# Performance work log

Measured on AMD Instinct MI355X. Metric: run time of the kernel, lower is better.

Reference implementation:

```python
import jax, jax.numpy as jnp
import numpy as np

B, N, E = 4, 4096, 65536
FIN, FOUT = 128, 64
ALPHA = 0.2          # LeakyReLU negative slope
NEG = -9e15          # mask value from original code


def setup_inputs() -> dict:
    key = jax.random.key(0)
    k1, k2, k3, k4 = jax.random.split(key, 4)
    h = jax.random.normal(k1, (B, N, FIN), dtype=jnp.float32)
    edge_index = jax.random.randint(k2, (B, 2, E), 0, N, dtype=jnp.int32)
    # Xavier-uniform-like params
    W = jax.random.uniform(k3, (FIN, FOUT), jnp.float32, -1.0, 1.0) * (1.414 * np.sqrt(6.0 / (FIN + FOUT)))
    a = jax.random.uniform(k4, (2 * FOUT, 1), jnp.float32, -1.0, 1.0) * (1.414 * np.sqrt(6.0 / (2 * FOUT + 1)))
    return {"h": h, "edge_index": edge_index, "W": W, "a": a}


def reference(h, edge_index, W, a):
    # Wh: [B, N, FOUT]
    Wh = jnp.einsum('bnf,fo->bno', h, W)
    Wh_flat = Wh.reshape(-1, FOUT)  # [B*N, FOUT]

    # Faithful to original: raw node ids (< N) index the flattened tensor,
    # i.e. edge features are gathered from batch 0's rows.
    src = edge_index[:, 0].reshape(-1)  # [B*E]
    tgt = edge_index[:, 1].reshape(-1)  # [B*E]
    a_input = jnp.concatenate([Wh_flat[src], Wh_flat[tgt]], axis=1)  # [B*E, 2*FOUT]
    e = (a_input @ a)[:, 0]  # [B*E]

    b_idx = jnp.repeat(jnp.arange(B), E)
    e_dense = jnp.zeros((B, N, N), e.dtype).at[b_idx, src, tgt].set(e)
    e_dense = jax.nn.leaky_relu(e_dense, ALPHA)

    attention = jnp.where(e_dense > 0, e_dense, NEG)
    attention = jax.nn.softmax(attention, axis=1)  # softmax over dim=1 as in original
    # dropout p=0.0 -> no-op

    h_prime = jnp.einsum('bmn,bnf->bmf', attention, Wh)  # [B, N, FOUT]
    return jax.nn.elu(h_prime)  # concat=True path
```

## Files before the change

kernel.cpp:

```cpp
#include <hip/hip_runtime.h>
#include <hip/hip_bf16.h>

#define BB 4
#define NN 4096
#define EE 65536
#define FIN 128
#define FOUT 64
#define CAP 64

__device__ __forceinline__ unsigned enc_f32(float f) {
    unsigned b = __float_as_uint(f);
    return (b & 0x80000000u) ? ~b : (b | 0x80000000u);
}
__device__ __forceinline__ float dec_f32(unsigned e) {
    unsigned b = (e & 0x80000000u) ? (e & 0x7FFFFFFFu) : ~e;
    return __uint_as_float(b);
}

__global__ void init_kernel(const float* __restrict__ W, const float* __restrict__ a,
                            int* __restrict__ deg, unsigned* __restrict__ Menc,
                            float* __restrict__ D, float* __restrict__ base,
                            float* __restrict__ Wa) {
    int tid = threadIdx.x;
    int gid = blockIdx.x * 256 + tid;
    deg[gid] = 0;
    Menc[gid] = 0u;
    D[gid] = 0.f;
    if (gid < BB * FOUT) base[gid] = 0.f;
    if (blockIdx.x == 0) {
        int half = tid >> 7, k = tid & 127;
        const float* wr = W + k * FOUT;
        const float* av = a + half * FOUT;
        float s = 0.f;
#pragma unroll 16
        for (int f = 0; f < FOUT; ++f) s += wr[f] * av[f];
        Wa[half * 128 + k] = s;
    }
}

__global__ void as_at_kernel(const float* __restrict__ h, const float* __restrict__ Wa,
                             float* __restrict__ as_, float* __restrict__ at_) {
    int tid = threadIdx.x;
    int lane = tid & 63;
    int n = blockIdx.x * 4 + (tid >> 6);
    float h0v = h[(long)n * FIN + lane];
    float h1v = h[(long)n * FIN + 64 + lane];
    float ps = h0v * Wa[lane] + h1v * Wa[64 + lane];
    float pt = h0v * Wa[128 + lane] + h1v * Wa[192 + lane];
    for (int off = 32; off; off >>= 1) {
        ps += __shfl_down(ps, off);
        pt += __shfl_down(pt, off);
    }
    if (lane == 0) { as_[n] = ps; at_[n] = pt; }
}

__global__ __launch_bounds__(256) void wh_kernel(const float* __restrict__ h,
                                                 const float* __restrict__ W,
                                                 float* __restrict__ Wh) {
    __shared__ float hs[32][132];
    __shared__ float Ws[128][64];
    int tid = threadIdx.x;
    long row0 = (long)blockIdx.x * 32;
    for (int i = tid; i < 2048; i += 256) {
        float4 v = ((const float4*)W)[i];
        int k = (i * 4) >> 6, c = (i * 4) & 63;
        *(float4*)&Ws[k][c] = v;
    }
    for (int i = tid; i < 1024; i += 256) {
        float4 v = ((const float4*)(h + row0 * FIN))[i];
        int r = (i * 4) >> 7, c = (i * 4) & 127;
        *(float4*)&hs[r][c] = v;
    }
    __syncthreads();
    int tx = tid & 15, ty = tid >> 4;
    int c0 = tx * 4, r0 = ty * 2;
    float acc[2][4] = {};
#pragma unroll
    for (int k = 0; k < 128; k += 4) {
        float4 w0 = *(const float4*)&Ws[k][c0];
        float4 w1 = *(const float4*)&Ws[k + 1][c0];
        float4 w2 = *(const float4*)&Ws[k + 2][c0];
        float4 w3 = *(const float4*)&Ws[k + 3][c0];
#pragma unroll
        for (int r = 0; r < 2; ++r) {
            float4 hv = *(const float4*)&hs[r0 + r][k];
            acc[r][0] += hv.x * w0.x + hv.y * w1.x + hv.z * w2.x + hv.w * w3.x;
            acc[r][1] += hv.x * w0.y + hv.y * w1.y + hv.z * w2.y + hv.w * w3.y;
            acc[r][2] += hv.x * w0.z + hv.y * w1.z + hv.z * w2.z + hv.w * w3.z;
            acc[r][3] += hv.x * w0.w + hv.y * w1.w + hv.z * w2.w + hv.w * w3.w;
        }
    }
#pragma unroll
    for (int r = 0; r < 2; ++r)
        *(float4*)&Wh[(row0 + r0 + r) * FOUT + c0] = *(float4*)&acc[r][0];
}

__global__ void edge_kernel(const int* __restrict__ ei, const float* __restrict__ as_,
                            const float* __restrict__ at_, unsigned* __restrict__ Menc,
                            int* __restrict__ deg, int* __restrict__ csr) {
    int idx = blockIdx.x * 256 + threadIdx.x;
    int b = idx >> 16;
    int j = idx & 65535;
    const int* eb = ei + (long)b * 2 * EE;
    int s = eb[j], t = eb[EE + j];
    float as_s = as_[s];
    float e = as_s + at_[t];
    if (e > 0.f) {
        int row = (b << 12) | s;
        atomicMax(&Menc[(b << 12) | t], enc_f32(as_s));
        int slot = atomicAdd(&deg[row], 1);
        if (slot < CAP) csr[row * CAP + slot] = t;
    }
}

__global__ void dedup_denom_kernel(int* __restrict__ deg, int* __restrict__ csr,
                                   const float* __restrict__ as_,
                                   const unsigned* __restrict__ Menc,
                                   float* __restrict__ D) {
    int tid = threadIdx.x;
    int lane = tid & 63;
    int row = blockIdx.x * 4 + (tid >> 6);
    int b = row >> 12, s = row & 4095;
    int draw = min(deg[row], CAP);
    int t = -1;
    if (lane < draw) t = csr[row * CAP + lane];
    bool dup = false;
    for (int k = 0; k < draw; ++k) {
        int tk = __shfl(t, k);
        if (k < lane && tk == t) dup = true;
    }
    bool keep = (lane < draw) && !dup;
    unsigned long long mask = __ballot(keep);
    int pfx = __popcll(mask & ((1ull << lane) - 1ull));
    if (keep) {
        csr[row * CAP + pfx] = t;
        float M = dec_f32(Menc[(b << 12) | t]);
        atomicAdd(&D[(b << 12) | t], expf(as_[s] - M));
    }
    if (lane == 0) deg[row] = __popcll(mask);
}

__global__ void base_kernel(const unsigned* __restrict__ Menc, const float* __restrict__ Wh,
                            float* __restrict__ base) {
    int bx = blockIdx.x;
    int b = bx >> 5, chunk = bx & 31;
    int f = threadIdx.x & 63, ty = threadIdx.x >> 6;
    float acc = 0.f;
    int t0 = chunk * (NN / 32);
    for (int t = t0 + ty; t < t0 + NN / 32; t += 4)
        if (Menc[(b << 12) | t] == 0u) acc += Wh[(((long)b << 12) | t) * FOUT + f];
    __shared__ float red[4][64];
    red[ty][f] = acc;
    __syncthreads();
    if (ty == 0)
        atomicAdd(&base[(b << 6) | f],
                  (red[0][f] + red[1][f] + red[2][f] + red[3][f]) * (1.0f / NN));
}

__global__ void gather_kernel(const int* __restrict__ deg, const int* __restrict__ csr,
                              const float* __restrict__ as_, const unsigned* __restrict__ Menc,
                              const float* __restrict__ D, const float* __restrict__ Wh,
                              const float* __restrict__ base, float* __restrict__ out) {
    int tid = threadIdx.x;
    int lane = tid & 63;
    int row = blockIdx.x * 4 + (tid >> 6);
    int b = row >> 12, s = row & 4095;
    int d = deg[row];
    float as_s = as_[s];
    float acc = 0.f;
    const int* cr = csr + row * CAP;
    const float* Whb = Wh + (((long)b << 12) * FOUT);
    for (int j = 0; j < d; ++j) {
        int t = cr[j];
        float M = dec_f32(Menc[(b << 12) | t]);
        float w = expf(as_s - M) / D[(b << 12) | t];
        acc += w * Whb[t * FOUT + lane];
    }
    float x = acc + base[(b << 6) | lane];
    out[(long)row * FOUT + lane] = x > 0.f ? x : expm1f(x);
}

extern "C" void kernel_launch(void* const* d_in, const int* in_sizes, int n_in,
                              void* d_out, int out_size, void* d_ws, size_t ws_size,
                              hipStream_t stream) {
    const float* h  = (const float*)d_in[0];
    const int*   ei = (const int*)d_in[1];
    const float* W  = (const float*)d_in[2];
    const float* a  = (const float*)d_in[3];
    float* out = (float*)d_out;

    char* ws = (char*)d_ws;
    float*    Wh   = (float*)(ws);
    int*      csr  = (int*)(ws + 4194304);
    int*      deg  = (int*)(ws + 8388608);
    unsigned* Menc = (unsigned*)(ws + 8454144);
    float*    D    = (float*)(ws + 8519680);
    float*    as_  = (float*)(ws + 8585216);
    float*    at_  = (float*)(ws + 8601600);
    float*    base = (float*)(ws + 8617984);
    float*    Wa   = (float*)(ws + 8619008);

    init_kernel<<<64, 256, 0, stream>>>(W, a, deg, Menc, D, base, Wa);
    wh_kernel<<<BB * NN / 32, 256, 0, stream>>>(h, W, Wh);
    as_at_kernel<<<NN / 4, 256, 0, stream>>>(h, Wa, as_, at_);
    edge_kernel<<<(BB * EE) / 256, 256, 0, stream>>>(ei, as_, at_, Menc, deg, csr);
    dedup_denom_kernel<<<(BB * NN) / 4, 256, 0, stream>>>(deg, csr, as_, Menc, D);
    base_kernel<<<BB * 32, 256, 0, stream>>>(Menc, Wh, base);
    gather_kernel<<<(BB * NN) / 4, 256, 0, stream>>>(deg, csr, as_, Menc, D, Wh, base, out);
}
```

Before: 79.47 us.

## Merge init, Wh and score kernels; fold base reduction into dedup kernel

After: 88.20 us. 1.11x slower.

```diff
diff --git a/kernel.cpp b/kernel.cpp
--- a/kernel.cpp
+++ b/kernel.cpp
@@ -17,82 +17,84 @@
     return __uint_as_float(b);
 }
 
-__global__ void init_kernel(const float* __restrict__ W, const float* __restrict__ a,
-                            int* __restrict__ deg, unsigned* __restrict__ Menc,
-                            float* __restrict__ D, float* __restrict__ base,
-                            float* __restrict__ Wa) {
+__global__ __launch_bounds__(256) void phase0_kernel(
+        const float* __restrict__ h, const float* __restrict__ W, const float* __restrict__ a,
+        float* __restrict__ Wh, int* __restrict__ deg, unsigned* __restrict__ Menc,
+        float* __restrict__ D, float* __restrict__ base,
+        float* __restrict__ as_, float* __restrict__ at_) {
+    __shared__ union {
+        struct { float hs[32][132]; float Ws[64][64]; } wh;
+        float Wa[256];
+    } smem;
     int tid = threadIdx.x;
-    int gid = blockIdx.x * 256 + tid;
-    deg[gid] = 0;
-    Menc[gid] = 0u;
-    D[gid] = 0.f;
-    if (gid < BB * FOUT) base[gid] = 0.f;
-    if (blockIdx.x == 0) {
-        int half = tid >> 7, k = tid & 127;
-        const float* wr = W + k * FOUT;
-        const float* av = a + half * FOUT;
-        float s = 0.f;
-#pragma unroll 16
-        for (int f = 0; f < FOUT; ++f) s += wr[f] * av[f];
-        Wa[half * 128 + k] = s;
-    }
-}
-
-__global__ void as_at_kernel(const float* __restrict__ h, const float* __restrict__ Wa,
-                             float* __restrict__ as_, float* __restrict__ at_) {
-    int tid = threadIdx.x;
-    int lane = tid & 63;
-    int n = blockIdx.x * 4 + (tid >> 6);
-    float h0v = h[(long)n * FIN + lane];
-    float h1v = h[(long)n * FIN + 64 + lane];
-    float ps = h0v * Wa[lane] + h1v * Wa[64 + lane];
-    float pt = h0v * Wa[128 + lane] + h1v * Wa[192 + lane];
-    for (int off = 32; off; off >>= 1) {
-        ps += __shfl_down(ps, off);
-        pt += __shfl_down(pt, off);
-    }
-    if (lane == 0) { as_[n] = ps; at_[n] = pt; }
-}
-
-__global__ __launch_bounds__(256) void wh_kernel(const float* __restrict__ h,
-                                                 const float* __restrict__ W,
-                                                 float* __restrict__ Wh) {
-    __shared__ float hs[32][132];
-    __shared__ float Ws[128][64];
-    int tid = threadIdx.x;
-    long row0 = (long)blockIdx.x * 32;
-    for (int i = tid; i < 2048; i += 256) {
-        float4 v = ((const float4*)W)[i];
-        int k = (i * 4) >> 6, c = (i * 4) & 63;
-        *(float4*)&Ws[k][c] = v;
-    }
-    for (int i = tid; i < 1024; i += 256) {
-        float4 v = ((const float4*)(h + row0 * FIN))[i];
-        int r = (i * 4) >> 7, c = (i * 4) & 127;
-        *(float4*)&hs[r][c] = v;
-    }
-    __syncthreads();
-    int tx = tid & 15, ty = tid >> 4;
-    int c0 = tx * 4, r0 = ty * 2;
-    float acc[2][4] = {};
-#pragma unroll
-    for (int k = 0; k < 128; k += 4) {
-        float4 w0 = *(const float4*)&Ws[k][c0];
-        float4 w1 = *(const float4*)&Ws[k + 1][c0];
-        float4 w2 = *(const float4*)&Ws[k + 2][c0];
-        float4 w3 = *(const float4*)&Ws[k + 3][c0];
+    int bid = blockIdx.x;
+    if (bid < 512) {
+        long row0 = (long)bid * 32;
+        for (int i = tid; i < 1024; i += 256) {
+            float4 v = ((const float4*)(h + row0 * FIN))[i];
+            int r = (i * 4) >> 7, c = (i * 4) & 127;
+            *(float4*)&smem.wh.hs[r][c] = v;
+        }
+        int tx = tid & 15, ty = tid >> 4;
+        int c0 = tx * 4, r0 = ty * 2;
+        float acc[2][4] = {};
+        for (int kk = 0; kk < 128; kk += 64) {
+            __syncthreads();
+            for (int i = tid; i < 1024; i += 256) {
+                float4 v = ((const float4*)(W + kk * FOUT))[i];
+                int k = (i * 4) >> 6, c = (i * 4) & 63;
+                *(float4*)&smem.wh.Ws[k][c] = v;
+            }
+            __syncthreads();
+#pragma unroll
+            for (int k = 0; k < 64; k += 4) {
+                float4 w0 = *(const float4*)&smem.wh.Ws[k][c0];
+                float4 w1 = *(const float4*)&smem.wh.Ws[k + 1][c0];
+                float4 w2 = *(const float4*)&smem.wh.Ws[k + 2][c0];
+                float4 w3 = *(const float4*)&smem.wh.Ws[k + 3][c0];
+#pragma unroll
+                for (int r = 0; r < 2; ++r) {
+                    float4 hv = *(const float4*)&smem.wh.hs[r0 + r][kk + k];
+                    acc[r][0] += hv.x * w0.x + hv.y * w1.x + hv.z * w2.x + hv.w * w3.x;
+                    acc[r][1] += hv.x * w0.y + hv.y * w1.y + hv.z * w2.y + hv.w * w3.y;
+                    acc[r][2] += hv.x * w0.z + hv.y * w1.z + hv.z * w2.z + hv.w * w3.z;
+                    acc[r][3] += hv.x * w0.w + hv.y * w1.w + hv.z * w2.w + hv.w * w3.w;
+                }
+            }
+        }
+#pragma unroll
+        for (int r = 0; r < 2; ++r)
+            *(float4*)&Wh[(row0 + r0 + r) * FOUT + c0] = *(float4*)&acc[r][0];
+    } else {
+        int local = bid - 512;
+        int gid2 = local * 256 + tid;
+        if (gid2 < BB * NN) { deg[gid2] = 0; Menc[gid2] = 0u; D[gid2] = 0.f; }
+        if (gid2 < BB * FOUT) base[gid2] = 0.f;
+        {
+            int half = tid >> 7, k = tid & 127;
+            const float* wr = W + k * FOUT;
+            const float* av = a + half * FOUT;
+            float s = 0.f;
+#pragma unroll
+            for (int f2 = 0; f2 < FOUT; ++f2) s += wr[f2] * av[f2];
+            smem.Wa[half * 128 + k] = s;
+        }
+        __syncthreads();
+        int lane = tid & 63, wv = tid >> 6;
 #pragma unroll
         for (int r = 0; r < 2; ++r) {
-            float4 hv = *(const float4*)&hs[r0 + r][k];
-            acc[r][0] += hv.x * w0.x + hv.y * w1.x + hv.z * w2.x + hv.w * w3.x;
-            acc[r][1] += hv.x * w0.y + hv.y * w1.y + hv.z * w2.y + hv.w * w3.y;
-            acc[r][2] += hv.x * w0.z + hv.y * w1.z + hv.z * w2.z + hv.w * w3.z;
-            acc[r][3] += hv.x * w0.w + hv.y * w1.w + hv.z * w2.w + hv.w * w3.w;
-        }
-    }
-#pragma unroll
-    for (int r = 0; r < 2; ++r)
-        *(float4*)&Wh[(row0 + r0 + r) * FOUT + c0] = *(float4*)&acc[r][0];
+            int n = local * 8 + wv * 2 + r;
+            float h0v = h[(long)n * FIN + lane];
+            float h1v = h[(long)n * FIN + 64 + lane];
+            float ps = h0v * smem.Wa[lane] + h1v * smem.Wa[64 + lane];
+            float pt = h0v * smem.Wa[128 + lane] + h1v * smem.Wa[192 + lane];
+            for (int off = 32; off; off >>= 1) {
+                ps += __shfl_down(ps, off);
+                pt += __shfl_down(pt, off);
+            }
+            if (lane == 0) { as_[n] = ps; at_[n] = pt; }
+        }
+    }
 }
 
 __global__ void edge_kernel(const int* __restrict__ ei, const float* __restrict__ as_,
@@ -104,8 +106,7 @@
     const int* eb = ei + (long)b * 2 * EE;
     int s = eb[j], t = eb[EE + j];
     float as_s = as_[s];
-    float e = as_s + at_[t];
-    if (e > 0.f) {
+    if (as_s + at_[t] > 0.f) {
         int row = (b << 12) | s;
         atomicMax(&Menc[(b << 12) | t], enc_f32(as_s));
         int slot = atomicAdd(&deg[row], 1);
@@ -113,10 +114,11 @@
     }
 }
 
-__global__ void dedup_denom_kernel(int* __restrict__ deg, int* __restrict__ csr,
-                                   const float* __restrict__ as_,
-                                   const unsigned* __restrict__ Menc,
-                                   float* __restrict__ D) {
+__global__ void phase2_kernel(int* __restrict__ deg, int* __restrict__ csr,
+                              const float* __restrict__ as_, const unsigned* __restrict__ Menc,
+                              float* __restrict__ D, const float* __restrict__ Wh,
+                              float* __restrict__ base) {
+    __shared__ float red[4][64];
     int tid = threadIdx.x;
     int lane = tid & 63;
     int row = blockIdx.x * 4 + (tid >> 6);
@@ -138,23 +140,20 @@
         atomicAdd(&D[(b << 12) | t], expf(as_[s] - M));
     }
     if (lane == 0) deg[row] = __popcll(mask);
-}
-
-__global__ void base_kernel(const unsigned* __restrict__ Menc, const float* __restrict__ Wh,
-                            float* __restrict__ base) {
-    int bx = blockIdx.x;
-    int b = bx >> 5, chunk = bx & 31;
-    int f = threadIdx.x & 63, ty = threadIdx.x >> 6;
-    float acc = 0.f;
-    int t0 = chunk * (NN / 32);
-    for (int t = t0 + ty; t < t0 + NN / 32; t += 4)
-        if (Menc[(b << 12) | t] == 0u) acc += Wh[(((long)b << 12) | t) * FOUT + f];
-    __shared__ float red[4][64];
-    red[ty][f] = acc;
-    __syncthreads();
-    if (ty == 0)
-        atomicAdd(&base[(b << 6) | f],
-                  (red[0][f] + red[1][f] + red[2][f] + red[3][f]) * (1.0f / NN));
+
+    if (blockIdx.x < 128) {
+        int bb = blockIdx.x >> 5, chunk = blockIdx.x & 31;
+        int f = tid & 63, ty = tid >> 6;
+        float acc = 0.f;
+        int t0 = chunk * (NN / 32);
+        for (int tt = t0 + ty; tt < t0 + NN / 32; tt += 4)
+            if (Menc[(bb << 12) | tt] == 0u) acc += Wh[(((long)bb << 12) | tt) * FOUT + f];
+        red[ty][f] = acc;
+        __syncthreads();
+        if (ty == 0)
+            atomicAdd(&base[(bb << 6) | f],
+                      (red[0][f] + red[1][f] + red[2][f] + red[3][f]) * (1.0f / NN));
+    }
 }
 
 __global__ void gather_kernel(const int* __restrict__ deg, const int* __restrict__ csr,
@@ -198,13 +197,9 @@
     float*    as_  = (float*)(ws + 8585216);
     float*    at_  = (float*)(ws + 8601600);
     float*    base = (float*)(ws + 8617984);
-    float*    Wa   = (float*)(ws + 8619008);
-
-    init_kernel<<<64, 256, 0, stream>>>(W, a, deg, Menc, D, base, Wa);
-    wh_kernel<<<BB * NN / 32, 256, 0, stream>>>(h, W, Wh);
-    as_at_kernel<<<NN / 4, 256, 0, stream>>>(h, Wa, as_, at_);
+
+    phase0_kernel<<<1024, 256, 0, stream>>>(h, W, a, Wh, deg, Menc, D, base, as_, at_);
     edge_kernel<<<(BB * EE) / 256, 256, 0, stream>>>(ei, as_, at_, Menc, deg, csr);
-    dedup_denom_kernel<<<(BB * NN) / 4, 256, 0, stream>>>(deg, csr, as_, Menc, D);
-    base_kernel<<<BB * 32, 256, 0, stream>>>(Menc, Wh, base);
+    phase2_kernel<<<(BB * NN) / 4, 256, 0, stream>>>(deg, csr, as_, Menc, D, Wh, base);
     gather_kernel<<<(BB * NN) / 4, 256, 0, stream>>>(deg, csr, as_, Menc, D, Wh, base, out);
 }
```
